# Performance work log

Hardware: AMD Instinct MI355X
Metric: run time of the kernel (lower is better)

## Reference

```python
import jax, jax.numpy as jnp
import numpy as np

GROUP = 32  # group_size from init


def setup_inputs() -> dict:
    key = jax.random.key(0)
    k1, k2, k3, k4, k5 = jax.random.split(key, 5)
    O, K = 4096, 4096
    B, S = 2, 2048
    num_groups = K // GROUP
    x = jax.random.normal(k1, (B, S, K), dtype=jnp.float32)
    # packed uint8 bytes (two 4-bit values per byte), stored as int32
    weight_packed = jax.random.randint(k2, (O, K // 2), 0, 256, dtype=jnp.int32)
    # realistic small positive scales and zero-points in [0, 15]
    scales = jax.random.uniform(k3, (O, num_groups), dtype=jnp.float32) * 0.02 + 1e-4
    zero_points = jax.random.uniform(k4, (O, num_groups), dtype=jnp.float32) * 15.0
    bias = jax.random.normal(k5, (O,), dtype=jnp.float32)
    return {"x": x, "weight_packed": weight_packed, "scales": scales,
            "zero_points": zero_points, "bias": bias}


def reference(x, weight_packed, scales, zero_points, bias):
    O, Kh = weight_packed.shape
    # unpack 4-bit values: even input index -> low nibble, odd -> high nibble
    low = weight_packed & 15
    high = (weight_packed >> 4) & 15
    q = jnp.stack([low, high], axis=-1).reshape(O, Kh * 2).astype(x.dtype)  # [O, K]
    # broadcast per-group scale/zero_point over the 32 elements of each group
    s = jnp.repeat(scales, GROUP, axis=1).astype(x.dtype)       # [O, K]
    z = jnp.repeat(zero_points, GROUP, axis=1).astype(x.dtype)  # [O, K]
    W = (q - z) * s  # dequantized weight [O, K]
    # F.linear: x @ W.T + bias
    return jnp.einsum('bsk,ok->bso', x, W) + bias
```

## Files before the change

### kernel.cpp

```cpp
#include <hip/hip_runtime.h>

typedef __attribute__((ext_vector_type(8))) short short8;
typedef __attribute__((ext_vector_type(4))) float f32x4;
typedef unsigned short u16;
typedef unsigned int u32;

#define BM 128
#define BN 128
#define BK 32
#define LDP 40

__device__ __forceinline__ u16 f2bf_rne(float f) {
    u32 u = __float_as_uint(f);
    return (u16)((u + 0x7fffu + ((u >> 16) & 1u)) >> 16);
}
__device__ __forceinline__ float bf2f(u16 b) { return __uint_as_float(((u32)b) << 16); }


__global__ __launch_bounds__(256)
void prep_w(const int* __restrict__ WP, const float* __restrict__ S,
            const float* __restrict__ Z, u16* __restrict__ Wd, int NG)
{
    const int tid = blockIdx.x * blockDim.x + threadIdx.x;
    const int o = tid / NG, g = tid % NG;
    const float s = S[o * NG + g];
    const float nzs = -Z[o * NG + g] * s;
    const int4* p = (const int4*)&WP[(size_t)(o * NG + g) * 16];
    __align__(16) u16 out[32];
    #pragma unroll
    for (int q4 = 0; q4 < 4; ++q4) {
        const int4 v4 = p[q4];
        const int vv[4] = {v4.x, v4.y, v4.z, v4.w};
        #pragma unroll
        for (int j = 0; j < 4; ++j) {
            const int v = vv[j];
            out[(q4 * 4 + j) * 2]     = f2bf_rne(fmaf((float)(v & 15), s, nzs));
            out[(q4 * 4 + j) * 2 + 1] = f2bf_rne(fmaf((float)((v >> 4) & 15), s, nzs));
        }
    }
    uint4* dst = (uint4*)&Wd[(size_t)tid * 32];
    const uint4* src = (const uint4*)out;
    dst[0] = src[0]; dst[1] = src[1]; dst[2] = src[2]; dst[3] = src[3];
}

__global__ __launch_bounds__(256)
void prep_x(const float* __restrict__ X, u16* __restrict__ Xh)
{
    const int tid = blockIdx.x * blockDim.x + threadIdx.x;
    const float4 v0 = ((const float4*)X)[tid * 2];
    const float4 v1 = ((const float4*)X)[tid * 2 + 1];
    const float f[8] = {v0.x, v0.y, v0.z, v0.w, v1.x, v1.y, v1.z, v1.w};
    __align__(16) u16 h[8];
    #pragma unroll
    for (int j = 0; j < 8; ++j) h[j] = f2bf_rne(f[j]);
    ((uint4*)Xh)[tid] = *(uint4*)h;
}


__global__ __launch_bounds__(256)
void gemm_q4(const u16* __restrict__ Xh, const u16* __restrict__ Wd,
             const float* __restrict__ Bi, float* __restrict__ C,
             int M, int N, int K)
{
    __shared__ __align__(16) u16 sA[BM * BK];
    __shared__ __align__(16) u16 sB[BN * BK];

    const int nbx = N / BN;
    const int nwg = gridDim.x;
    const int cpx = nwg >> 3;
    const int bid = blockIdx.x;
    const int swz = (bid & 7) * cpx + (bid >> 3);
    const int bx = swz % nbx, by = swz / nbx;
    const int brow = by * BM, bcol = bx * BN;

    const int t = threadIdx.x;
    const int lane = t & 63;
    const int wid = t >> 6;
    const int wr = wid >> 1, wc = wid & 1;
    const int fr = lane & 15;
    const int kslot = lane >> 4;

    const int r0 = t >> 2, sl = t & 3;

    f32x4 acc[4][4];
    #pragma unroll
    for (int m = 0; m < 4; ++m)
        #pragma unroll
        for (int n = 0; n < 4; ++n) acc[m][n] = (f32x4)0.f;

#define GLDS(gptr, ldsbase_bytes)                                                   \
    __builtin_amdgcn_global_load_lds(                                               \
        (const __attribute__((address_space(1))) u32*)(gptr),                       \
        (__attribute__((address_space(3))) u32*)(ldsbase_bytes), 16, 0, 0)

    const int nkt = K / BK;
    for (int kt = 0; kt < nkt; ++kt) {
        const int kc = kt * BK;
        {
            char* bA = (char*)sA + wid * 1024;
            char* bB = (char*)sB + wid * 1024;
            const u16* gA0 = Xh + (size_t)(brow + r0) * K + kc + sl * 8;
            const u16* gA1 = Xh + (size_t)(brow + 64 + r0) * K + kc + sl * 8;
            const u16* gB0 = Wd + (size_t)(bcol + r0) * K + kc + sl * 8;
            const u16* gB1 = Wd + (size_t)(bcol + 64 + r0) * K + kc + sl * 8;
            GLDS(gA0, bA);
            GLDS(gA1, bA + 4096);
            GLDS(gB0, bB);
            GLDS(gB1, bB + 4096);
        }
        __syncthreads();

        short8 a[4], b[4];
        #pragma unroll
        for (int m = 0; m < 4; ++m) {
            const int row = wr * 64 + m * 16 + fr;
            a[m] = *(const short8*)&sA[row * BK + kslot * 8];
        }
        #pragma unroll
        for (int n = 0; n < 4; ++n) {
            const int row = wc * 64 + n * 16 + fr;
            b[n] = *(const short8*)&sB[row * BK + kslot * 8];
        }
        #pragma unroll
        for (int m = 0; m < 4; ++m)
            #pragma unroll
            for (int n = 0; n < 4; ++n)
                acc[m][n] = __builtin_amdgcn_mfma_f32_16x16x32_bf16(a[m], b[n], acc[m][n], 0, 0, 0);
        __syncthreads();
    }

    const int row4 = (lane >> 4) << 2;
    const int col = lane & 15;
    #pragma unroll
    for (int n = 0; n < 4; ++n) {
        const int gc = bcol + wc * 64 + n * 16 + col;
        const float bb = Bi[gc];
        #pragma unroll
        for (int m = 0; m < 4; ++m) {
            const int gr = brow + wr * 64 + m * 16 + row4;
            #pragma unroll
            for (int i = 0; i < 4; ++i)
                C[(size_t)(gr + i) * N + gc] = acc[m][n][i] + bb;
        }
    }
#undef GLDS
}


__global__ __launch_bounds__(256, 2)
void q4_gemm_fused(const float* __restrict__ X, const int* __restrict__ WP,
                   const float* __restrict__ S, const float* __restrict__ Z,
                   const float* __restrict__ Bi, float* __restrict__ C,
                   int M, int N, int K, int NG)
{
    __shared__ __align__(16) u16 sa_hi[BM][LDP];
    __shared__ __align__(16) u16 sa_lo[BM][LDP];
    __shared__ __align__(16) u16 sb_hi[BN][LDP];
    __shared__ __align__(16) u16 sb_lo[BN][LDP];

    const int nbx = N / BN;
    const int bx = blockIdx.x % nbx;
    const int by = blockIdx.x / nbx;
    const int brow = by * BM, bcol = bx * BN;

    const int t = threadIdx.x;
    const int lane = t & 63;
    const int wid = t >> 6;
    const int wr = wid >> 1, wc = wid & 1;
    const int xc4 = t & 7, xr0 = t >> 3;
    const int wrow = t >> 1, whalf = t & 1;
    const int Kh = K >> 1;

    f32x4 acc[4][4];
    #pragma unroll
    for (int m = 0; m < 4; ++m)
        #pragma unroll
        for (int n = 0; n < 4; ++n) acc[m][n] = (f32x4)0.f;

    const int fr = lane & 15;
    const int k8 = (lane >> 4) << 3;

    const int nkt = K / BK;
    for (int kt = 0; kt < nkt; ++kt) {
        #pragma unroll
        for (int p = 0; p < 4; ++p) {
            const int r = xr0 + p * 32;
            const float4 v = *(const float4*)&X[(size_t)(brow + r) * K + kt * BK + xc4 * 4];
            u16 h[4], l[4];
            const float f[4] = {v.x, v.y, v.z, v.w};
            #pragma unroll
            for (int j = 0; j < 4; ++j) {
                h[j] = f2bf_rne(f[j]);
                l[j] = f2bf_rne(f[j] - bf2f(h[j]));
            }
            *(ushort4*)&sa_hi[r][xc4 * 4] = *(ushort4*)h;
            *(ushort4*)&sa_lo[r][xc4 * 4] = *(ushort4*)l;
        }
        {
            const int n = bcol + wrow;
            const float s = S[n * NG + kt];
            const float z = Z[n * NG + kt];
            const float nzs = -z * s;
            const int4* pp = (const int4*)&WP[(size_t)n * Kh + kt * 16 + whalf * 8];
            const int4 p0 = pp[0], p1 = pp[1];
            const int vals[8] = {p0.x, p0.y, p0.z, p0.w, p1.x, p1.y, p1.z, p1.w};
            __align__(16) u16 hi[16], lo[16];
            #pragma unroll
            for (int j = 0; j < 8; ++j) {
                const int v = vals[j];
                const float w0 = fmaf((float)(v & 15), s, nzs);
                const float w1 = fmaf((float)((v >> 4) & 15), s, nzs);
                hi[2 * j] = f2bf_rne(w0); lo[2 * j] = f2bf_rne(w0 - bf2f(hi[2 * j]));
                hi[2 * j + 1] = f2bf_rne(w1); lo[2 * j + 1] = f2bf_rne(w1 - bf2f(hi[2 * j + 1]));
            }
            #pragma unroll
            for (int q = 0; q < 4; ++q) {
                *(ushort4*)&sb_hi[wrow][whalf * 16 + q * 4] = *(ushort4*)&hi[q * 4];
                *(ushort4*)&sb_lo[wrow][whalf * 16 + q * 4] = *(ushort4*)&lo[q * 4];
            }
        }
        __syncthreads();

        short8 ah[4], al[4], bh[4], bl[4];
        #pragma unroll
        for (int m = 0; m < 4; ++m) {
            ah[m] = *(const short8*)&sa_hi[wr * 64 + m * 16 + fr][k8];
            al[m] = *(const short8*)&sa_lo[wr * 64 + m * 16 + fr][k8];
        }
        #pragma unroll
        for (int n = 0; n < 4; ++n) {
            bh[n] = *(const short8*)&sb_hi[wc * 64 + n * 16 + fr][k8];
            bl[n] = *(const short8*)&sb_lo[wc * 64 + n * 16 + fr][k8];
        }
        #pragma unroll
        for (int m = 0; m < 4; ++m)
            #pragma unroll
            for (int n = 0; n < 4; ++n) {
                acc[m][n] = __builtin_amdgcn_mfma_f32_16x16x32_bf16(ah[m], bh[n], acc[m][n], 0, 0, 0);
                acc[m][n] = __builtin_amdgcn_mfma_f32_16x16x32_bf16(ah[m], bl[n], acc[m][n], 0, 0, 0);
                acc[m][n] = __builtin_amdgcn_mfma_f32_16x16x32_bf16(al[m], bh[n], acc[m][n], 0, 0, 0);
            }
        __syncthreads();
    }

    const int row4 = (lane >> 4) << 2;
    const int col = lane & 15;
    #pragma unroll
    for (int n = 0; n < 4; ++n) {
        const int gc = bcol + wc * 64 + n * 16 + col;
        const float bb = Bi[gc];
        #pragma unroll
        for (int m = 0; m < 4; ++m) {
            const int gr = brow + wr * 64 + m * 16 + row4;
            #pragma unroll
            for (int i = 0; i < 4; ++i)
                C[(size_t)(gr + i) * N + gc] = acc[m][n][i] + bb;
        }
    }
}


extern "C" void kernel_launch(void* const* d_in, const int* in_sizes, int n_in,
                              void* d_out, int out_size, void* d_ws, size_t ws_size,
                              hipStream_t stream)
{
    const float* X  = (const float*)d_in[0];
    const int*   WP = (const int*)d_in[1];
    const float* S  = (const float*)d_in[2];
    const float* Z  = (const float*)d_in[3];
    const float* Bi = (const float*)d_in[4];
    float* C = (float*)d_out;

    const int O  = in_sizes[4];
    const int NG = in_sizes[2] / O;
    const int K  = NG * 32;
    const int M  = in_sizes[0] / K;

    const size_t needW = (size_t)O * K * 2;
    const size_t needX = (size_t)M * K * 2;
    const size_t need = needW + needX;

    if (ws_size >= need) {
        u16* Wd  = (u16*)d_ws;
        u16* Xhp = Wd + (size_t)O * K;

        prep_w<<<(O * NG) / 256, 256, 0, stream>>>(WP, S, Z, Wd, NG);
        prep_x<<<(M * K / 8) / 256, 256, 0, stream>>>(X, Xhp);

        dim3 grid((M / BM) * (O / BN));
        gemm_q4<<<grid, 256, 0, stream>>>(Xhp, Wd, Bi, C, M, O, K);
    } else {
        dim3 grid((M / BM) * (O / BN));
        q4_gemm_fused<<<grid, 256, 0, stream>>>(X, WP, S, Z, Bi, C, M, O, K, NG);
    }
}
```

Before: 373.2 us.

## Use 256x256 tiles with 4-stage async LDS pipeline and swizzled layout

Rewrites the bf16 GEMM to use 256x256 output tiles with 512 threads (8 waves, 8x4 MFMA tiles per wave). A four-deep LDS ring is filled by global_load_lds, with explicit vmcnt waits and barriers so loads overlap MFMA work instead of a full sync each k-step. The LDS layout is XOR-swizzled to cut bank conflicts, and s_setprio raises wave priority around the MFMA block. The larger tile gives more data reuse but raises register pressure and LDS use to 128KB per block, and it yields only 256 blocks for this problem, which limits occupancy.

```diff
diff --git a/kernel.cpp b/kernel.cpp
--- a/kernel.cpp
+++ b/kernel.cpp
@@ -5,9 +5,10 @@
 typedef unsigned short u16;
 typedef unsigned int u32;
 
-#define BM 128
-#define BN 128
+#define BM 256
+#define BN 256
 #define BK 32
+#define NBUF 4
 #define LDP 40
 
 __device__ __forceinline__ u16 f2bf_rne(float f) {
@@ -57,13 +58,18 @@
 }
 
 
-__global__ __launch_bounds__(256)
+#define GLDS(gptr, ldsbase)                                                         \
+    __builtin_amdgcn_global_load_lds(                                               \
+        (const __attribute__((address_space(1))) u32*)(gptr),                       \
+        (__attribute__((address_space(3))) u32*)(ldsbase), 16, 0, 0)
+
+__global__ __launch_bounds__(512, 2)
 void gemm_q4(const u16* __restrict__ Xh, const u16* __restrict__ Wd,
              const float* __restrict__ Bi, float* __restrict__ C,
              int M, int N, int K)
 {
-    __shared__ __align__(16) u16 sA[BM * BK];
-    __shared__ __align__(16) u16 sB[BN * BK];
+    __shared__ __align__(16) u16 sA[NBUF * 8192];
+    __shared__ __align__(16) u16 sB[NBUF * 8192];
 
     const int nbx = N / BN;
     const int nwg = gridDim.x;
@@ -76,75 +82,98 @@
     const int t = threadIdx.x;
     const int lane = t & 63;
     const int wid = t >> 6;
-    const int wr = wid >> 1, wc = wid & 1;
+    const int wr = wid >> 2;
+    const int wcn = wid & 3;
     const int fr = lane & 15;
-    const int kslot = lane >> 4;
-
-    const int r0 = t >> 2, sl = t & 3;
-
-    f32x4 acc[4][4];
-    #pragma unroll
-    for (int m = 0; m < 4; ++m)
+    const int ps8 = (((lane >> 4) ^ ((lane >> 2) & 3)) << 3);
+
+    const int srow = wid * 16 + (lane >> 2);
+    const int schunk = ((lane & 3) ^ ((lane >> 4) & 3)) * 8;
+    const u16* srcA0 = Xh + (size_t)(brow + srow) * K + schunk;
+    const u16* srcA1 = Xh + (size_t)(brow + 128 + srow) * K + schunk;
+    const u16* srcB0 = Wd + (size_t)(bcol + srow) * K + schunk;
+    const u16* srcB1 = Wd + (size_t)(bcol + 128 + srow) * K + schunk;
+
+    f32x4 acc[8][4];
+    #pragma unroll
+    for (int m = 0; m < 8; ++m)
         #pragma unroll
         for (int n = 0; n < 4; ++n) acc[m][n] = (f32x4)0.f;
 
-#define GLDS(gptr, ldsbase_bytes)                                                   \
-    __builtin_amdgcn_global_load_lds(                                               \
-        (const __attribute__((address_space(1))) u32*)(gptr),                       \
-        (__attribute__((address_space(3))) u32*)(ldsbase_bytes), 16, 0, 0)
-
     const int nkt = K / BK;
+
+#define STAGE(bufi, kt)                                                   \
+    do {                                                                  \
+        const size_t ko = (size_t)(kt) * BK;                              \
+        char* baA = (char*)sA + (bufi) * 16384 + wid * 1024;              \
+        char* baB = (char*)sB + (bufi) * 16384 + wid * 1024;              \
+        GLDS(srcA0 + ko, baA);                                            \
+        GLDS(srcA1 + ko, baA + 8192);                                     \
+        GLDS(srcB0 + ko, baB);                                            \
+        GLDS(srcB1 + ko, baB + 8192);                                     \
+    } while (0)
+
+    STAGE(0, 0);
+    STAGE(1, 1);
+    STAGE(2, 2);
+    STAGE(3, 3);
+    asm volatile("s_waitcnt vmcnt(12)" ::: "memory");
+    __builtin_amdgcn_s_barrier();
+
     for (int kt = 0; kt < nkt; ++kt) {
-        const int kc = kt * BK;
-        {
-            char* bA = (char*)sA + wid * 1024;
-            char* bB = (char*)sB + wid * 1024;
-            const u16* gA0 = Xh + (size_t)(brow + r0) * K + kc + sl * 8;
-            const u16* gA1 = Xh + (size_t)(brow + 64 + r0) * K + kc + sl * 8;
-            const u16* gB0 = Wd + (size_t)(bcol + r0) * K + kc + sl * 8;
-            const u16* gB1 = Wd + (size_t)(bcol + 64 + r0) * K + kc + sl * 8;
-            GLDS(gA0, bA);
-            GLDS(gA1, bA + 4096);
-            GLDS(gB0, bB);
-            GLDS(gB1, bB + 4096);
-        }
-        __syncthreads();
-
-        short8 a[4], b[4];
-        #pragma unroll
-        for (int m = 0; m < 4; ++m) {
-            const int row = wr * 64 + m * 16 + fr;
-            a[m] = *(const short8*)&sA[row * BK + kslot * 8];
+        const int cur = kt & 3;
+        const u16* bufA = sA + cur * 8192;
+        const u16* bufB = sB + cur * 8192;
+
+        short8 a[8], b[4];
+        #pragma unroll
+        for (int m = 0; m < 8; ++m) {
+            const int row = wr * 128 + m * 16 + fr;
+            a[m] = *(const short8*)&bufA[row * 32 + ps8];
         }
         #pragma unroll
         for (int n = 0; n < 4; ++n) {
-            const int row = wc * 64 + n * 16 + fr;
-            b[n] = *(const short8*)&sB[row * BK + kslot * 8];
-        }
-        #pragma unroll
-        for (int m = 0; m < 4; ++m)
+            const int row = wcn * 64 + n * 16 + fr;
+            b[n] = *(const short8*)&bufB[row * 32 + ps8];
+        }
+
+        asm volatile("s_waitcnt lgkmcnt(0)" ::: "memory");
+        __builtin_amdgcn_s_barrier();
+
+        if (kt + 4 < nkt) STAGE(cur, kt + 4);
+
+        __builtin_amdgcn_s_setprio(1);
+        #pragma unroll
+        for (int m = 0; m < 8; ++m)
             #pragma unroll
             for (int n = 0; n < 4; ++n)
                 acc[m][n] = __builtin_amdgcn_mfma_f32_16x16x32_bf16(a[m], b[n], acc[m][n], 0, 0, 0);
-        __syncthreads();
+        __builtin_amdgcn_s_setprio(0);
+
+        if (kt + 4 < nkt)      asm volatile("s_waitcnt vmcnt(12)" ::: "memory");
+        else if (kt + 3 < nkt) asm volatile("s_waitcnt vmcnt(8)"  ::: "memory");
+        else if (kt + 2 < nkt) asm volatile("s_waitcnt vmcnt(4)"  ::: "memory");
+        else if (kt + 1 < nkt) asm volatile("s_waitcnt vmcnt(0)"  ::: "memory");
+        __builtin_amdgcn_s_barrier();
     }
 
     const int row4 = (lane >> 4) << 2;
     const int col = lane & 15;
     #pragma unroll
     for (int n = 0; n < 4; ++n) {
-        const int gc = bcol + wc * 64 + n * 16 + col;
+        const int gc = bcol + wcn * 64 + n * 16 + col;
         const float bb = Bi[gc];
         #pragma unroll
-        for (int m = 0; m < 4; ++m) {
-            const int gr = brow + wr * 64 + m * 16 + row4;
+        for (int m = 0; m < 8; ++m) {
+            const int gr = brow + wr * 128 + m * 16 + row4;
             #pragma unroll
             for (int i = 0; i < 4; ++i)
                 C[(size_t)(gr + i) * N + gc] = acc[m][n][i] + bb;
         }
     }
+}
+#undef STAGE
 #undef GLDS
-}
 
 
 __global__ __launch_bounds__(256, 2)
@@ -153,15 +182,15 @@
                    const float* __restrict__ Bi, float* __restrict__ C,
                    int M, int N, int K, int NG)
 {
-    __shared__ __align__(16) u16 sa_hi[BM][LDP];
-    __shared__ __align__(16) u16 sa_lo[BM][LDP];
-    __shared__ __align__(16) u16 sb_hi[BN][LDP];
-    __shared__ __align__(16) u16 sb_lo[BN][LDP];
-
-    const int nbx = N / BN;
+    __shared__ __align__(16) u16 sa_hi[128][LDP];
+    __shared__ __align__(16) u16 sa_lo[128][LDP];
+    __shared__ __align__(16) u16 sb_hi[128][LDP];
+    __shared__ __align__(16) u16 sb_lo[128][LDP];
+
+    const int nbx = N / 128;
     const int bx = blockIdx.x % nbx;
     const int by = blockIdx.x / nbx;
-    const int brow = by * BM, bcol = bx * BN;
+    const int brow = by * 128, bcol = bx * 128;
 
     const int t = threadIdx.x;
     const int lane = t & 63;
@@ -180,12 +209,12 @@
     const int fr = lane & 15;
     const int k8 = (lane >> 4) << 3;
 
-    const int nkt = K / BK;
+    const int nkt = K / 32;
     for (int kt = 0; kt < nkt; ++kt) {
         #pragma unroll
         for (int p = 0; p < 4; ++p) {
             const int r = xr0 + p * 32;
-            const float4 v = *(const float4*)&X[(size_t)(brow + r) * K + kt * BK + xc4 * 4];
+            const float4 v = *(const float4*)&X[(size_t)(brow + r) * K + kt * 32 + xc4 * 4];
             u16 h[4], l[4];
             const float f[4] = {v.x, v.y, v.z, v.w};
             #pragma unroll
@@ -280,7 +309,7 @@
     const size_t needX = (size_t)M * K * 2;
     const size_t need = needW + needX;
 
-    if (ws_size >= need) {
+    if (ws_size >= need && (M % BM) == 0 && (O % BN) == 0) {
         u16* Wd  = (u16*)d_ws;
         u16* Xhp = Wd + (size_t)O * K;
 
@@ -288,9 +317,9 @@
         prep_x<<<(M * K / 8) / 256, 256, 0, stream>>>(X, Xhp);
 
         dim3 grid((M / BM) * (O / BN));
-        gemm_q4<<<grid, 256, 0, stream>>>(Xhp, Wd, Bi, C, M, O, K);
+        gemm_q4<<<grid, 512, 0, stream>>>(Xhp, Wd, Bi, C, M, O, K);
     } else {
-        dim3 grid((M / BM) * (O / BN));
+        dim3 grid((M / 128) * (O / 128));
         q4_gemm_fused<<<grid, 256, 0, stream>>>(X, WP, S, Z, Bi, C, M, O, K, NG);
     }
 }
```

Result: faster. 307.1 us (-17.7%).
